# Kernel tuning notes

Hardware: AMD Instinct MI355X
Metric: run time of the kernel (lower is better)

## Reference

```python
import jax, jax.numpy as jnp
import numpy as np

N, E = 20000, 640000
F_IN, H, T = 64, 256, 64  # in_channels = T, edge_attr dim = T -> EdgeConv MLP in = 3*T


def _lin(key, fan_in, fan_out):
    k1, k2 = jax.random.split(key)
    s = 1.0 / np.sqrt(fan_in)
    W = jax.random.uniform(k1, (fan_in, fan_out), jnp.float32, -s, s)
    b = jax.random.uniform(k2, (fan_out,), jnp.float32, -s, s)
    return W, b


def setup_inputs() -> dict:
    key = jax.random.key(0)
    ks = jax.random.split(key, 12)
    x = jax.random.normal(ks[0], (N, F_IN), jnp.float32)
    edge_index = jax.random.randint(ks[1], (2, E), 0, N, jnp.int32)
    edge_attr = jax.random.normal(ks[2], (E, T), jnp.float32)
    conv1_W, conv1_b = _lin(ks[3], F_IN, H)
    e_W1, e_b1 = _lin(ks[4], 3 * T, H)
    e_W2, e_b2 = _lin(ks[5], H, H)
    conv2_W, conv2_b = _lin(ks[6], 2 * H, H)
    conv3_W, conv3_b = _lin(ks[7], H, F_IN)
    lin1_W, lin1_b = _lin(ks[8], 2 * F_IN, F_IN)
    lin2_W, lin2_b = _lin(ks[9], F_IN, 128)
    lin3_W, lin3_b = _lin(ks[10], 128, 32)
    lin4_W, lin4_b = _lin(ks[11], 32, 2)
    return dict(x=x, edge_index=edge_index, edge_attr=edge_attr,
                conv1_W=conv1_W, conv1_b=conv1_b,
                e_W1=e_W1, e_b1=e_b1, e_W2=e_W2, e_b2=e_b2,
                conv2_W=conv2_W, conv2_b=conv2_b,
                conv3_W=conv3_W, conv3_b=conv3_b,
                lin1_W=lin1_W, lin1_b=lin1_b, lin2_W=lin2_W, lin2_b=lin2_b,
                lin3_W=lin3_W, lin3_b=lin3_b, lin4_W=lin4_W, lin4_b=lin4_b)


def reference(x, edge_index, edge_attr,
              conv1_W, conv1_b, e_W1, e_b1, e_W2, e_b2,
              conv2_W, conv2_b, conv3_W, conv3_b,
              lin1_W, lin1_b, lin2_W, lin2_b, lin3_W, lin3_b, lin4_W, lin4_b):
    n = x.shape[0]
    src, dst = edge_index[0], edge_index[1]
    # GCN symmetric norm with self-loops (deg counted on dst, +1 for self-loop)
    deg = jax.ops.segment_sum(jnp.ones_like(src, jnp.float32), dst, num_segments=n) + 1.0
    dis = jax.lax.rsqrt(deg)

    def gcn(h, W, b):
        hw = h @ W
        msg = hw[src] * (dis[src] * dis[dst])[:, None]
        # self-loop contribution: norm = dis[i]^2
        return jax.ops.segment_sum(msg, dst, num_segments=n) + hw * (dis * dis)[:, None] + b

    out1 = jax.nn.relu(gcn(x, conv1_W, conv1_b))
    # EdgeConv: MLP(cat[x_i, x_j, edge_attr]) with max aggregation onto dst (x_i = target)
    m = jnp.concatenate([x[dst], x[src], edge_attr], axis=1)      # [E, 3T]
    m = jax.nn.relu(m @ e_W1 + e_b1) @ e_W2 + e_b2                 # [E, H]
    agg = jax.ops.segment_max(m, dst, num_segments=n)
    agg = jnp.where(jnp.isfinite(agg), agg, 0.0)                   # nodes with no in-edges
    out_e1 = jax.nn.relu(agg)

    out2 = jax.nn.relu(gcn(jnp.concatenate([out1, out_e1], axis=1), conv2_W, conv2_b))
    out3 = jax.nn.relu(gcn(out2, conv3_W, conv3_b))
    h = jnp.concatenate([x, out3], axis=1)
    h = jax.nn.softplus(h @ lin1_W + lin1_b)
    h = jax.nn.softplus(h @ lin2_W + lin2_b)
    h = jax.nn.softplus(h @ lin3_W + lin3_b)
    h = h @ lin4_W + lin4_b                                        # [N, 2]
    return (h[:, 0], h[:, 1])
```

## Files before the change

### kernel.cpp

```cpp
#include <hip/hip_runtime.h>
#include <stdint.h>

typedef __bf16 bf16x8 __attribute__((ext_vector_type(8)));
typedef float f32x4 __attribute__((ext_vector_type(4)));
typedef unsigned short u16x8 __attribute__((ext_vector_type(8)));
typedef unsigned long long ull_t;
typedef unsigned short ushort_t;

#define DEV __device__ __forceinline__

DEV unsigned short f2bf(float f) {
  __bf16 b = (__bf16)f;
  return __builtin_bit_cast(unsigned short, b);
}

DEV float bf2f(unsigned short b) { return __uint_as_float((unsigned int)b << 16); }

DEV f32x4 zero4() { f32x4 z = {0.f, 0.f, 0.f, 0.f}; return z; }

DEV float softplusf(float v) { return (v > 15.f) ? v : log1pf(expf(v)); }

DEV void pack_dev(const float* __restrict__ W, unsigned short* __restrict__ P,
                  int Ncols, int permk, int idx) {
  int j = idx & 7;
  int lane = (idx >> 3) & 63;
  int rest = idx >> 9;
  int NT = Ncols >> 4;
  int nt = rest % NT;
  int kt = rest / NT;
  int k = kt * 32 + ((j >> 2) * 16) + ((lane >> 4) * 4) + (j & 3);
  if (permk) k = (k & ~63) | ((k & 3) << 4) | ((k >> 2) & 15);
  int col = nt * 16 + (lane & 15);
  P[idx] = f2bf(W[(size_t)k * Ncols + col]);
}

__global__ __launch_bounds__(256) void k_prologue(
    const float* __restrict__ c1W, unsigned short* __restrict__ p_c1,
    const float* __restrict__ eW1, unsigned short* __restrict__ p_e1,
    const float* __restrict__ eW2, unsigned short* __restrict__ p_e2,
    const float* __restrict__ c2W, unsigned short* __restrict__ p_c2,
    const float* __restrict__ c3W, unsigned short* __restrict__ p_c3,
    const float* __restrict__ x, ushort_t* __restrict__ xb,
    const int* __restrict__ dsts, int* __restrict__ degi,
    int n4, int E, int nb_cvt) {
  const int b = blockIdx.x;
  const int tid = threadIdx.x;
  if (b < 64) {
    pack_dev(c1W, p_c1, 256, 0, b * 256 + tid);
  } else if (b < 256) {
    pack_dev(eW1, p_e1, 256, 0, (b - 64) * 256 + tid);
  } else if (b < 512) {
    pack_dev(eW2, p_e2, 256, 1, (b - 256) * 256 + tid);
  } else if (b < 1024) {
    pack_dev(c2W, p_c2, 256, 0, (b - 512) * 256 + tid);
  } else if (b < 1088) {
    pack_dev(c3W, p_c3, 64, 0, (b - 1024) * 256 + tid);
  } else if (b < 1088 + nb_cvt) {
    int i = (b - 1088) * 256 + tid;
    if (i < n4) {
      float4 v = *(const float4*)(x + (size_t)i * 4);
      ushort4 u;
      u.x = f2bf(v.x); u.y = f2bf(v.y); u.z = f2bf(v.z); u.w = f2bf(v.w);
      *(ushort4*)(xb + (size_t)i * 4) = u;
    }
  } else {
    int i = (b - 1088 - nb_cvt) * 256 + tid;
    if (i < E) atomicAdd(&degi[dsts[i]], 1);
  }
}

__global__ __launch_bounds__(1024) void k_scan_dis(const int* __restrict__ degi,
                                                   int* __restrict__ ptr,
                                                   float* __restrict__ dis, int n) {
  __shared__ int part[1024];
  const int tid = threadIdx.x;
  const int chunk = (n + 1023) / 1024;
  const int b = tid * chunk;
  const int e2 = min(n, b + chunk);
  int s = 0;
  for (int i = b; i < e2; ++i) {
    int d = degi[i];
    dis[i] = rsqrtf((float)d + 1.0f);
    s += d;
  }
  part[tid] = s;
  __syncthreads();
  for (int off = 1; off < 1024; off <<= 1) {
    int val = (tid >= off) ? part[tid - off] : 0;
    __syncthreads();
    part[tid] += val;
    __syncthreads();
  }
  int run = (tid == 0) ? 0 : part[tid - 1];
  for (int i = b; i < e2; ++i) {
    ptr[i] = run;
    run += degi[i];
  }
  if (tid == 1023) ptr[n] = run;
}

__global__ void k_fill(const int* __restrict__ srcs, const int* __restrict__ dsts,
                       const int* __restrict__ ptr, const float* __restrict__ dis,
                       int* __restrict__ fillc,
                       int2* __restrict__ sc_s, int* __restrict__ dst_s,
                       int* __restrict__ perm_s, int E) {
  int e = blockIdx.x * 256 + threadIdx.x;
  if (e >= E) return;
  int d = dsts[e];
  int s = srcs[e];
  int pos = ptr[d] + atomicAdd(&fillc[d], 1);
  float c = dis[s] * dis[d];
  sc_s[pos] = make_int2(s, __float_as_int(c));
  dst_s[pos] = d;
  perm_s[pos] = e;
}

template <int COLS, bool FINALIZE, bool INBF16>
__global__ __launch_bounds__(256) void k_gather_agg(
    const void* __restrict__ featv, const int2* __restrict__ sc,
    const int* __restrict__ ptr, const float* __restrict__ dis,
    const void* __restrict__ hwv, const float* __restrict__ bias,
    float* __restrict__ out, int n) {
  constexpr int V = COLS / 64;
  const int v = blockIdx.x * 4 + (threadIdx.x >> 6);
  if (v >= n) return;
  const int lane = threadIdx.x & 63;
  const int beg = ptr[v], end = ptr[v + 1];

  auto loadrow = [&](int s, float* f) {
    if constexpr (INBF16) {
      const ushort_t* feat = (const ushort_t*)featv;
      if constexpr (V == 4) {
        ushort4 u = *(const ushort4*)(feat + (size_t)s * COLS + lane * 4);
        f[0] = bf2f(u.x); f[1] = bf2f(u.y); f[2] = bf2f(u.z); f[3] = bf2f(u.w);
      } else {
        f[0] = bf2f(feat[(size_t)s * COLS + lane]);
      }
    } else {
      const float* feat = (const float*)featv;
      if constexpr (V == 4) {
        float4 q = *(const float4*)(feat + (size_t)s * COLS + lane * 4);
        f[0] = q.x; f[1] = q.y; f[2] = q.z; f[3] = q.w;
      } else {
        f[0] = feat[(size_t)s * COLS + lane];
      }
    }
  };

  float acc[V];
#pragma unroll
  for (int i = 0; i < V; ++i) acc[i] = 0.f;
  const int cnt = end - beg;
  const int2* scp = sc + beg;
  int i = 0;
  for (; i + 4 <= cnt; i += 4) {
    int2 s0 = scp[i], s1 = scp[i + 1], s2 = scp[i + 2], s3 = scp[i + 3];
    float f0[V], f1[V], f2[V], f3[V];
    loadrow(s0.x, f0); loadrow(s1.x, f1); loadrow(s2.x, f2); loadrow(s3.x, f3);
    float c0 = __int_as_float(s0.y), c1 = __int_as_float(s1.y);
    float c2 = __int_as_float(s2.y), c3 = __int_as_float(s3.y);
#pragma unroll
    for (int j = 0; j < V; ++j)
      acc[j] += f0[j] * c0 + f1[j] * c1 + f2[j] * c2 + f3[j] * c3;
  }
  for (; i < cnt; ++i) {
    int2 s0 = scp[i];
    float c0 = __int_as_float(s0.y);
    float f0[V];
    loadrow(s0.x, f0);
#pragma unroll
    for (int j = 0; j < V; ++j) acc[j] += f0[j] * c0;
  }
  float* op = out + (size_t)v * COLS + lane * V;
  if constexpr (FINALIZE) {
    const float dv = dis[v];
    float d2 = dv * dv;
    float h[V];
    if constexpr (INBF16) {
      const ushort_t* hw = (const ushort_t*)hwv;
      if constexpr (V == 4) {
        ushort4 u = *(const ushort4*)(hw + (size_t)v * COLS + lane * 4);
        h[0] = bf2f(u.x); h[1] = bf2f(u.y); h[2] = bf2f(u.z); h[3] = bf2f(u.w);
      } else {
        h[0] = bf2f(hw[(size_t)v * COLS + lane]);
      }
    } else {
      const float* hw = (const float*)hwv;
      if constexpr (V == 4) {
        float4 q = *(const float4*)(hw + (size_t)v * COLS + lane * 4);
        h[0] = q.x; h[1] = q.y; h[2] = q.z; h[3] = q.w;
      } else {
        h[0] = hw[(size_t)v * COLS + lane];
      }
    }
#pragma unroll
    for (int i2 = 0; i2 < V; ++i2)
      acc[i2] = fmaxf(acc[i2] + h[i2] * d2 + bias[lane * V + i2], 0.f);
  }
  if constexpr (V == 4) {
    *(float4*)op = make_float4(acc[0], acc[1], acc[2], acc[3]);
  } else {
    op[0] = acc[0];
  }
}

template <int K, int NOUT, bool COMPOSE, bool RELUBIAS, bool OUTBF16>
__global__ __launch_bounds__(256, 2) void gcn_gemm(
    const float* __restrict__ inA, const float* __restrict__ inB,
    const float* __restrict__ dis,
    const unsigned short* __restrict__ Wp, const float* __restrict__ bias,
    void* __restrict__ outv, int out_stride, int nrows) {
  constexpr int NT = NOUT / 16;
  constexpr int NTW = NOUT / 64;
  __shared__ unsigned short s_in[64 * K];
  const int tid = threadIdx.x;
  const int r0 = blockIdx.x * 64;

  constexpr int C4R = K / 4;
  for (int idx = tid; idx < 64 * C4R; idx += 256) {
    int row = idx / C4R;
    int rem = idx - row * C4R;
    int grow = r0 + row;
    float4 v = make_float4(0.f, 0.f, 0.f, 0.f);
    if (grow < nrows) {
      v = *(const float4*)&inA[(size_t)grow * K + rem * 4];
      if constexpr (COMPOSE) {
        float d = dis[grow];
        d *= d;
        float4 w2 = *(const float4*)&inB[(size_t)grow * K + rem * 4];
        v.x += w2.x * d; v.y += w2.y * d; v.z += w2.z * d; v.w += w2.w * d;
      }
    }
    ushort4 b;
    b.x = f2bf(v.x); b.y = f2bf(v.y); b.z = f2bf(v.z); b.w = f2bf(v.w);
    *(ushort4*)&s_in[row * K + ((rem ^ (row & 7)) * 4)] = b;
  }
  __syncthreads();

  const int lane = tid & 63, wid = tid >> 6;
  const int lr = lane & 15, lg = lane >> 4;
  f32x4 acc[4][NTW];
#pragma unroll
  for (int m = 0; m < 4; ++m)
#pragma unroll
    for (int n2 = 0; n2 < NTW; ++n2) acc[m][n2] = zero4();

#pragma unroll
  for (int kt = 0; kt < K / 32; ++kt) {
    bf16x8 a[4];
#pragma unroll
    for (int m = 0; m < 4; ++m) {
      int rA = m * 16 + lr;
      int c1 = (kt * 8 + lg) ^ (rA & 7);
      int c2 = (kt * 8 + lg + 4) ^ (rA & 7);
      union { bf16x8 v; ull_t q[2]; } u;
      u.q[0] = *(const ull_t*)&s_in[rA * K + c1 * 4];
      u.q[1] = *(const ull_t*)&s_in[rA * K + c2 * 4];
      a[m] = u.v;
    }
#pragma unroll
    for (int n2 = 0; n2 < NTW; ++n2) {
      int nt = wid * NTW + n2;
      bf16x8 b = *(const bf16x8*)&Wp[(((kt * NT + nt) * 64 + lane) * 8)];
#pragma unroll
      for (int m = 0; m < 4; ++m)
        acc[m][n2] = __builtin_amdgcn_mfma_f32_16x16x32_bf16(a[m], b, acc[m][n2], 0, 0, 0);
    }
  }

#pragma unroll
  for (int n2 = 0; n2 < NTW; ++n2) {
    int col = (wid * NTW + n2) * 16 + lr;
    float bv = 0.f;
    if (RELUBIAS) bv = bias[col];
#pragma unroll
    for (int m = 0; m < 4; ++m) {
#pragma unroll
      for (int r = 0; r < 4; ++r) {
        int grow = r0 + m * 16 + lg * 4 + r;
        if (grow < nrows) {
          float v = acc[m][n2][r];
          if (RELUBIAS) v = fmaxf(v + bv, 0.f);
          if constexpr (OUTBF16) {
            ((ushort_t*)outv)[(size_t)grow * out_stride + col] = f2bf(v);
          } else {
            ((float*)outv)[(size_t)grow * out_stride + col] = v;
          }
        }
      }
    }
  }
}

__global__ __launch_bounds__(512, 4) void k_fused(
    const float* __restrict__ x, const float* __restrict__ ea,
    const int2* __restrict__ sc_s, const int* __restrict__ dst_s,
    const int* __restrict__ perm_s,
    const unsigned short* __restrict__ W1p, const float* __restrict__ b1,
    const unsigned short* __restrict__ W2p, const float* __restrict__ b2,
    float* __restrict__ h2, int E, int nbE,
    const ushort_t* __restrict__ xb, const int* __restrict__ ptr,
    float* __restrict__ agg1, int n) {
  const int tid = threadIdx.x;
  const int lane = tid & 63, wid = tid >> 6;

  if (blockIdx.x >= nbE) {
    const int v = (blockIdx.x - nbE) * 8 + wid;
    if (v >= n) return;
    const int beg = ptr[v], end = ptr[v + 1];
    float acc = 0.f;
    const int cnt = end - beg;
    const int2* scp = sc_s + beg;
    int i = 0;
    for (; i + 4 <= cnt; i += 4) {
      int2 s0 = scp[i], s1 = scp[i + 1], s2 = scp[i + 2], s3 = scp[i + 3];
      float f0 = bf2f(xb[(size_t)s0.x * 64 + lane]);
      float f1 = bf2f(xb[(size_t)s1.x * 64 + lane]);
      float f2 = bf2f(xb[(size_t)s2.x * 64 + lane]);
      float f3 = bf2f(xb[(size_t)s3.x * 64 + lane]);
      acc += f0 * __int_as_float(s0.y) + f1 * __int_as_float(s1.y) +
             f2 * __int_as_float(s2.y) + f3 * __int_as_float(s3.y);
    }
    for (; i < cnt; ++i) {
      int2 s0 = scp[i];
      acc += bf2f(xb[(size_t)s0.x * 64 + lane]) * __int_as_float(s0.y);
    }
    agg1[(size_t)v * 64 + lane] = acc;
    return;
  }

  __shared__ unsigned short s_buf[256 * 136];
  __shared__ int s_src[128], s_dst[128], s_perm[128];
  __shared__ ull_t s_mask[2];
  const int e0 = blockIdx.x * 128;
  if (tid < 128) {
    int e = e0 + tid;
    s_src[tid] = (e < E) ? sc_s[e].x : 0;
    s_dst[tid] = (e < E) ? dst_s[e] : 0;
    s_perm[tid] = (e < E) ? perm_s[e] : 0;
  }
  __syncthreads();
  if (wid < 2) {
    int r = wid * 64 + lane;
    bool chg = (r > 0) && (s_dst[r] != s_dst[r - 1]);
    ull_t m = __ballot(chg);
    if (lane == 0) s_mask[wid] = m;
  }
#pragma unroll
  for (int seg = 0; seg < 3; ++seg) {
#pragma unroll
    for (int it = 0; it < 4; ++it) {
      int idx = it * 512 + tid;
      int ei = idx >> 4;
      int q = idx & 15;
      const float* row;
      if (seg == 0) row = x + (unsigned)s_dst[ei] * 64u;
      else if (seg == 1) row = x + (unsigned)s_src[ei] * 64u;
      else row = ea + (unsigned)s_perm[ei] * 64u;
      float4 v = make_float4(0.f, 0.f, 0.f, 0.f);
      if (e0 + ei < E) v = *(const float4*)(row + q * 4);
      ushort4 b;
      b.x = f2bf(v.x); b.y = f2bf(v.y); b.z = f2bf(v.z); b.w = f2bf(v.w);
      int chunk = (seg * 16 + q) ^ (ei & 7);
      *(ushort4*)&s_buf[ei * 192 + chunk * 4] = b;
    }
  }
  __syncthreads();

  const int wr = wid >> 2;
  const int wc = wid & 3;
  const int lr = lane & 15, lg = lane >> 4;
  f32x4 acc[4][4];
#pragma unroll
  for (int m = 0; m < 4; ++m)
#pragma unroll
    for (int n2 = 0; n2 < 4; ++n2) acc[m][n2] = zero4();

#pragma unroll
  for (int kt = 0; kt < 6; ++kt) {
    bf16x8 a[4];
#pragma unroll
    for (int m = 0; m < 4; ++m) {
      int rA = wr * 64 + m * 16 + lr;
      int rr = rA & 7;
      union { bf16x8 v; ull_t q[2]; } u;
      u.q[0] = *(const ull_t*)&s_buf[rA * 192 + ((kt * 8 + lg) ^ rr) * 4];
      u.q[1] = *(const ull_t*)&s_buf[rA * 192 + ((kt * 8 + lg + 4) ^ rr) * 4];
      a[m] = u.v;
    }
#pragma unroll
    for (int n2 = 0; n2 < 4; ++n2) {
      int nt = wc * 4 + n2;
      bf16x8 b = *(const bf16x8*)&W1p[(((kt * 16 + nt) * 64 + lane) * 8)];
#pragma unroll
      for (int m = 0; m < 4; ++m)
        acc[m][n2] = __builtin_amdgcn_mfma_f32_16x16x32_bf16(a[m], b, acc[m][n2], 0, 0, 0);
    }
  }
  __syncthreads();

  {
    float b1v[4];
#pragma unroll
    for (int n2 = 0; n2 < 4; ++n2) b1v[n2] = b1[(wc * 4 + n2) * 16 + lr];
#pragma unroll
    for (int m = 0; m < 4; ++m) {
#pragma unroll
      for (int r = 0; r < 4; ++r) {
        int row = wr * 64 + m * 16 + lg * 4 + r;
        union { ushort_t h[4]; ull_t q; } pk;
        pk.h[0] = f2bf(fmaxf(acc[m][0][r] + b1v[0], 0.f));
        pk.h[1] = f2bf(fmaxf(acc[m][1][r] + b1v[1], 0.f));
        pk.h[2] = f2bf(fmaxf(acc[m][2][r] + b1v[2], 0.f));
        pk.h[3] = f2bf(fmaxf(acc[m][3][r] + b1v[3], 0.f));
        int chunk = (wc * 16 + lr) ^ (row & 7);
        *(ull_t*)&s_buf[row * 256 + chunk * 4] = pk.q;
      }
    }
  }
  __syncthreads();

#pragma unroll
  for (int m = 0; m < 4; ++m)
#pragma unroll
    for (int n2 = 0; n2 < 4; ++n2) acc[m][n2] = zero4();
#pragma unroll
  for (int kt = 0; kt < 8; ++kt) {
    bf16x8 a[4];
#pragma unroll
    for (int m = 0; m < 4; ++m) {
      int rA = wr * 64 + m * 16 + lr;
      int rr = rA & 7;
      union { bf16x8 v; ull_t q[2]; } u;
      u.q[0] = *(const ull_t*)&s_buf[rA * 256 + ((kt * 8 + lg) ^ rr) * 4];
      u.q[1] = *(const ull_t*)&s_buf[rA * 256 + ((kt * 8 + lg + 4) ^ rr) * 4];
      a[m] = u.v;
    }
#pragma unroll
    for (int n2 = 0; n2 < 4; ++n2) {
      int nt = wc * 4 + n2;
      bf16x8 b = *(const bf16x8*)&W2p[(((kt * 16 + nt) * 64 + lane) * 8)];
#pragma unroll
      for (int m = 0; m < 4; ++m)
        acc[m][n2] = __builtin_amdgcn_mfma_f32_16x16x32_bf16(a[m], b, acc[m][n2], 0, 0, 0);
    }
  }
  __syncthreads();

#pragma unroll
  for (int n2 = 0; n2 < 4; ++n2) {
    int col = (wc * 4 + n2) * 16 + lr;
    float bv = b2[col];
#pragma unroll
    for (int m = 0; m < 4; ++m) {
      int rbase = wr * 64 + m * 16 + lg * 4;
      union { ushort_t h[4]; ull_t q; } pk;
#pragma unroll
      for (int r = 0; r < 4; ++r) {
        int row = rbase + r;
        float v = (e0 + row < E) ? fmaxf(acc[m][n2][r] + bv, 0.f) : 0.f;
        pk.h[r] = f2bf(v);
      }
      *(ull_t*)&s_buf[col * 136 + rbase] = pk.q;
    }
  }
  __syncthreads();

  {
    const int col = tid & 255;
    const int half = tid >> 8;
    const int rbeg = half * 64;
    const ull_t mask = s_mask[half];
    unsigned int run = 0;
    int segstart = rbeg;
#pragma unroll
    for (int i = 0; i < 8; ++i) {
      u16x8 pack = *(const u16x8*)&s_buf[col * 136 + rbeg + i * 8];
#pragma unroll
      for (int r2 = 0; r2 < 8; ++r2) {
        int rloc = i * 8 + r2;
        if ((mask >> rloc) & 1ull) {
          if (run > 0)
            atomicMax((int*)h2 + ((unsigned)s_dst[segstart] * 512u + 256u + col),
                      (int)(run << 16));
          run = 0;
          segstart = rbeg + rloc;
        }
        run = max(run, (unsigned int)pack[r2]);
      }
    }
    if (run > 0)
      atomicMax((int*)h2 + ((unsigned)s_dst[segstart] * 512u + 256u + col),
                (int)(run << 16));
  }
}

__global__ __launch_bounds__(256) void k_head(
    const float* __restrict__ x, const float* __restrict__ out3,
    const float* __restrict__ W1, const float* __restrict__ b1,
    const float* __restrict__ W2, const float* __restrict__ b2,
    const float* __restrict__ W3, const float* __restrict__ b3,
    const float* __restrict__ W4, const float* __restrict__ b4,
    float* __restrict__ out, int n) {
  __shared__ float sW1[128 * 64];
  __shared__ float sW3[128 * 32];
  __shared__ float sW4[32 * 2];
  __shared__ float sb1[64], sb2[128], sb3[32], sb4[2];
  __shared__ float sbuf[4][352];
  const int tid = threadIdx.x;
  for (int i = tid; i < 128 * 64; i += 256) sW1[i] = W1[i];
  for (int i = tid; i < 128 * 32; i += 256) sW3[i] = W3[i];
  if (tid < 64) sW4[tid] = W4[tid];
  if (tid < 64) sb1[tid] = b1[tid];
  if (tid < 128) sb2[tid] = b2[tid];
  if (tid < 32) sb3[tid] = b3[tid];
  if (tid < 2) sb4[tid] = b4[tid];
  __syncthreads();
  const int wid = tid >> 6, lane = tid & 63;
  float* B = sbuf[wid];
  const int per = gridDim.x * 4;
  const int iters = (n + per - 1) / per;
  for (int it = 0; it < iters; ++it) {
    const int node = it * per + blockIdx.x * 4 + wid;
    const bool act = node < n;
    if (act) {
      B[lane] = x[(size_t)node * 64 + lane];
      B[64 + lane] = out3[(size_t)node * 64 + lane];
    }
    __syncthreads();
    if (act) {
      float o = sb1[lane];
#pragma unroll 8
      for (int k = 0; k < 128; ++k) o += B[k] * sW1[k * 64 + lane];
      B[128 + lane] = softplusf(o);
    }
    __syncthreads();
    if (act) {
      float o0 = sb2[lane], o1 = sb2[64 + lane];
#pragma unroll 8
      for (int k = 0; k < 64; ++k) {
        float v = B[128 + k];
        o0 += v * W2[k * 128 + lane];
        o1 += v * W2[k * 128 + 64 + lane];
      }
      B[192 + lane] = softplusf(o0);
      B[256 + lane] = softplusf(o1);
    }
    __syncthreads();
    if (act && lane < 32) {
      float o = sb3[lane];
#pragma unroll 8
      for (int k = 0; k < 128; ++k) o += B[192 + k] * sW3[k * 32 + lane];
      B[320 + lane] = softplusf(o);
    }
    __syncthreads();
    if (act && lane < 2) {
      float o = sb4[lane];
#pragma unroll
      for (int k = 0; k < 32; ++k) o += B[320 + k] * sW4[k * 2 + lane];
      out[(size_t)lane * n + node] = o;
    }
    __syncthreads();
  }
}

static inline size_t alignup(size_t v) { return (v + 255) & ~(size_t)255; }

extern "C" void kernel_launch(void* const* d_in, const int* in_sizes, int n_in,
                              void* d_out, int out_size, void* d_ws, size_t ws_size,
                              hipStream_t stream) {
  const float* x = (const float*)d_in[0];
  const int* ei = (const int*)d_in[1];
  const float* ea = (const float*)d_in[2];
  const float* c1W = (const float*)d_in[3];
  const float* c1b = (const float*)d_in[4];
  const float* eW1 = (const float*)d_in[5];
  const float* eb1 = (const float*)d_in[6];
  const float* eW2 = (const float*)d_in[7];
  const float* eb2 = (const float*)d_in[8];
  const float* c2W = (const float*)d_in[9];
  const float* c2b = (const float*)d_in[10];
  const float* c3W = (const float*)d_in[11];
  const float* c3b = (const float*)d_in[12];
  const float* l1W = (const float*)d_in[13];
  const float* l1b = (const float*)d_in[14];
  const float* l2W = (const float*)d_in[15];
  const float* l2b = (const float*)d_in[16];
  const float* l3W = (const float*)d_in[17];
  const float* l3b = (const float*)d_in[18];
  const float* l4W = (const float*)d_in[19];
  const float* l4b = (const float*)d_in[20];
  const int n = in_sizes[0] / 64;
  const int E = in_sizes[1] / 2;
  const int* srcs = ei;
  const int* dsts = ei + E;

  char* w = (char*)d_ws;
  auto alloc = [&](size_t bytes) {
    char* p = w;
    w += alignup(bytes);
    return p;
  };
  float* dis = (float*)alloc((size_t)n * 4);
  int* degi = (int*)alloc((size_t)n * 4);
  int* ptr = (int*)alloc((size_t)(n + 1) * 4);
  int* fillc = (int*)alloc((size_t)n * 4);
  int2* sc_s = (int2*)alloc((size_t)E * 8);
  int* dst_s = (int*)alloc((size_t)E * 4);
  int* perm_s = (int*)alloc((size_t)E * 4);
  float* agg1 = (float*)alloc((size_t)n * 64 * 4);
  float* h2 = (float*)alloc((size_t)n * 512 * 4);
  ushort_t* hw2b = (ushort_t*)alloc((size_t)n * 256 * 2);
  float* out2 = (float*)alloc((size_t)n * 256 * 4);
  ushort_t* hw3b = (ushort_t*)alloc((size_t)n * 64 * 2);
  float* out3 = (float*)alloc((size_t)n * 64 * 4);
  ushort_t* xb = (ushort_t*)alloc((size_t)n * 64 * 2);
  unsigned short* p_c1 = (unsigned short*)alloc(64 * 256 * 2);
  unsigned short* p_e1 = (unsigned short*)alloc(192 * 256 * 2);
  unsigned short* p_e2 = (unsigned short*)alloc(256 * 256 * 2);
  unsigned short* p_c2 = (unsigned short*)alloc(512 * 256 * 2);
  unsigned short* p_c3 = (unsigned short*)alloc(256 * 64 * 2);

  hipMemsetAsync(degi, 0, (size_t)n * 4, stream);
  hipMemsetAsync(fillc, 0, (size_t)n * 4, stream);
  hipMemsetAsync(h2, 0, (size_t)n * 512 * 4, stream);

  const int n4 = n * 16;
  const int nb_cvt = (n4 + 255) / 256;
  const int nb_deg = (E + 255) / 256;
  k_prologue<<<1088 + nb_cvt + nb_deg, 256, 0, stream>>>(
      c1W, p_c1, eW1, p_e1, eW2, p_e2, c2W, p_c2, c3W, p_c3,
      x, xb, dsts, degi, n4, E, nb_cvt);

  k_scan_dis<<<1, 1024, 0, stream>>>(degi, ptr, dis, n);
  k_fill<<<(E + 255) / 256, 256, 0, stream>>>(srcs, dsts, ptr, dis, fillc,
                                              sc_s, dst_s, perm_s, E);

  const int ablocks = (n + 3) / 4;
  const int gblocks = (n + 63) / 64;
  const int nbE = (E + 127) / 128;
  const int nbG = (n + 7) / 8;

  k_fused<<<nbE + nbG, 512, 0, stream>>>(x, ea, sc_s, dst_s, perm_s,
                                         p_e1, eb1, p_e2, eb2, h2, E, nbE,
                                         xb, ptr, agg1, n);

  gcn_gemm<64, 256, true, true, false><<<gblocks, 256, 0, stream>>>(
      agg1, x, dis, p_c1, c1b, h2, 512, n);

  gcn_gemm<512, 256, false, false, true><<<gblocks, 256, 0, stream>>>(
      h2, nullptr, nullptr, p_c2, nullptr, hw2b, 256, n);
  k_gather_agg<256, true, true><<<ablocks, 256, 0, stream>>>(
      hw2b, sc_s, ptr, dis, hw2b, c2b, out2, n);

  gcn_gemm<256, 64, false, false, true><<<gblocks, 256, 0, stream>>>(
      out2, nullptr, nullptr, p_c3, nullptr, hw3b, 64, n);
  k_gather_agg<64, true, true><<<ablocks, 256, 0, stream>>>(
      hw3b, sc_s, ptr, dis, hw3b, c3b, out3, n);

  k_head<<<1250, 256, 0, stream>>>(x, out3, l1W, l1b, l2W, l2b, l3W, l3b, l4W, l4b,
                                   (float*)d_out, n);
}
```

Baseline: 617.2 us.

## Split h2 into bf16 GCN half and fp32 edge half, un-fuse agg kernel

Removes the side-branch from the fused EdgeConv kernel. The GCN-1 aggregation now runs as a separate k_gather_agg launch, and conv1 writes its output as bf16 into its own buffer. The EdgeConv atomics target a separate fp32 buffer half the former width, so the memset and traffic on the combined 512-wide fp32 h2 shrink. A new mixed-input GEMM reads the bf16 and fp32 halves and converts them while staging into shared memory. This adds a launch and gives up the overlap that came from co-scheduling the aggregation blocks with the edge blocks.

```diff
diff --git a/kernel.cpp b/kernel.cpp
--- a/kernel.cpp
+++ b/kernel.cpp
@@ -292,47 +292,91 @@
   }
 }
 
-__global__ __launch_bounds__(512, 4) void k_fused(
+__global__ __launch_bounds__(256, 2) void gcn_gemm_mix(
+    const ushort_t* __restrict__ h2a, const float* __restrict__ h2b,
+    const unsigned short* __restrict__ Wp, ushort_t* __restrict__ outv,
+    int nrows) {
+  constexpr int K = 512, NT = 16, NTW = 4;
+  __shared__ unsigned short s_in[64 * K];
+  const int tid = threadIdx.x;
+  const int r0 = blockIdx.x * 64;
+
+  for (int idx = tid; idx < 64 * 128; idx += 256) {
+    int row = idx >> 7;
+    int rem = idx & 127;
+    int grow = r0 + row;
+    ushort4 b = make_ushort4(0, 0, 0, 0);
+    if (grow < nrows) {
+      if (rem < 64) {
+        b = *(const ushort4*)&h2a[(size_t)grow * 256 + rem * 4];
+      } else {
+        float4 v = *(const float4*)&h2b[(size_t)grow * 256 + (rem - 64) * 4];
+        b.x = f2bf(v.x); b.y = f2bf(v.y); b.z = f2bf(v.z); b.w = f2bf(v.w);
+      }
+    }
+    *(ushort4*)&s_in[row * K + ((rem ^ (row & 7)) * 4)] = b;
+  }
+  __syncthreads();
+
+  const int lane = tid & 63, wid = tid >> 6;
+  const int lr = lane & 15, lg = lane >> 4;
+  f32x4 acc[4][NTW];
+#pragma unroll
+  for (int m = 0; m < 4; ++m)
+#pragma unroll
+    for (int n2 = 0; n2 < NTW; ++n2) acc[m][n2] = zero4();
+
+#pragma unroll
+  for (int kt = 0; kt < K / 32; ++kt) {
+    bf16x8 a[4];
+#pragma unroll
+    for (int m = 0; m < 4; ++m) {
+      int rA = m * 16 + lr;
+      int c1 = (kt * 8 + lg) ^ (rA & 7);
+      int c2 = (kt * 8 + lg + 4) ^ (rA & 7);
+      union { bf16x8 v; ull_t q[2]; } u;
+      u.q[0] = *(const ull_t*)&s_in[rA * K + c1 * 4];
+      u.q[1] = *(const ull_t*)&s_in[rA * K + c2 * 4];
+      a[m] = u.v;
+    }
+#pragma unroll
+    for (int n2 = 0; n2 < NTW; ++n2) {
+      int nt = wid * NTW + n2;
+      bf16x8 b = *(const bf16x8*)&Wp[(((kt * NT + nt) * 64 + lane) * 8)];
+#pragma unroll
+      for (int m = 0; m < 4; ++m)
+        acc[m][n2] = __builtin_amdgcn_mfma_f32_16x16x32_bf16(a[m], b, acc[m][n2], 0, 0, 0);
+    }
+  }
+
+#pragma unroll
+  for (int n2 = 0; n2 < NTW; ++n2) {
+    int col = (wid * NTW + n2) * 16 + lr;
+#pragma unroll
+    for (int m = 0; m < 4; ++m) {
+#pragma unroll
+      for (int r = 0; r < 4; ++r) {
+        int grow = r0 + m * 16 + lg * 4 + r;
+        if (grow < nrows)
+          outv[(size_t)grow * 256 + col] = f2bf(acc[m][n2][r]);
+      }
+    }
+  }
+}
+
+__global__ __launch_bounds__(512, 4) void k_edgeconv(
     const float* __restrict__ x, const float* __restrict__ ea,
     const int2* __restrict__ sc_s, const int* __restrict__ dst_s,
     const int* __restrict__ perm_s,
     const unsigned short* __restrict__ W1p, const float* __restrict__ b1,
     const unsigned short* __restrict__ W2p, const float* __restrict__ b2,
-    float* __restrict__ h2, int E, int nbE,
-    const ushort_t* __restrict__ xb, const int* __restrict__ ptr,
-    float* __restrict__ agg1, int n) {
-  const int tid = threadIdx.x;
-  const int lane = tid & 63, wid = tid >> 6;
-
-  if (blockIdx.x >= nbE) {
-    const int v = (blockIdx.x - nbE) * 8 + wid;
-    if (v >= n) return;
-    const int beg = ptr[v], end = ptr[v + 1];
-    float acc = 0.f;
-    const int cnt = end - beg;
-    const int2* scp = sc_s + beg;
-    int i = 0;
-    for (; i + 4 <= cnt; i += 4) {
-      int2 s0 = scp[i], s1 = scp[i + 1], s2 = scp[i + 2], s3 = scp[i + 3];
-      float f0 = bf2f(xb[(size_t)s0.x * 64 + lane]);
-      float f1 = bf2f(xb[(size_t)s1.x * 64 + lane]);
-      float f2 = bf2f(xb[(size_t)s2.x * 64 + lane]);
-      float f3 = bf2f(xb[(size_t)s3.x * 64 + lane]);
-      acc += f0 * __int_as_float(s0.y) + f1 * __int_as_float(s1.y) +
-             f2 * __int_as_float(s2.y) + f3 * __int_as_float(s3.y);
-    }
-    for (; i < cnt; ++i) {
-      int2 s0 = scp[i];
-      acc += bf2f(xb[(size_t)s0.x * 64 + lane]) * __int_as_float(s0.y);
-    }
-    agg1[(size_t)v * 64 + lane] = acc;
-    return;
-  }
-
+    float* __restrict__ h2b, int E) {
   __shared__ unsigned short s_buf[256 * 136];
   __shared__ int s_src[128], s_dst[128], s_perm[128];
   __shared__ ull_t s_mask[2];
+  const int tid = threadIdx.x;
   const int e0 = blockIdx.x * 128;
+  const int lane = tid & 63, wid = tid >> 6;
   if (tid < 128) {
     int e = e0 + tid;
     s_src[tid] = (e < E) ? sc_s[e].x : 0;
@@ -481,7 +525,7 @@
         int rloc = i * 8 + r2;
         if ((mask >> rloc) & 1ull) {
           if (run > 0)
-            atomicMax((int*)h2 + ((unsigned)s_dst[segstart] * 512u + 256u + col),
+            atomicMax((int*)h2b + ((unsigned)s_dst[segstart] * 256u + col),
                       (int)(run << 16));
           run = 0;
           segstart = rbeg + rloc;
@@ -490,7 +534,7 @@
       }
     }
     if (run > 0)
-      atomicMax((int*)h2 + ((unsigned)s_dst[segstart] * 512u + 256u + col),
+      atomicMax((int*)h2b + ((unsigned)s_dst[segstart] * 256u + col),
                 (int)(run << 16));
   }
 }
@@ -609,7 +653,8 @@
   int* dst_s = (int*)alloc((size_t)E * 4);
   int* perm_s = (int*)alloc((size_t)E * 4);
   float* agg1 = (float*)alloc((size_t)n * 64 * 4);
-  float* h2 = (float*)alloc((size_t)n * 512 * 4);
+  ushort_t* h2a = (ushort_t*)alloc((size_t)n * 256 * 2);
+  float* h2b = (float*)alloc((size_t)n * 256 * 4);
   ushort_t* hw2b = (ushort_t*)alloc((size_t)n * 256 * 2);
   float* out2 = (float*)alloc((size_t)n * 256 * 4);
   ushort_t* hw3b = (ushort_t*)alloc((size_t)n * 64 * 2);
@@ -623,7 +668,7 @@
 
   hipMemsetAsync(degi, 0, (size_t)n * 4, stream);
   hipMemsetAsync(fillc, 0, (size_t)n * 4, stream);
-  hipMemsetAsync(h2, 0, (size_t)n * 512 * 4, stream);
+  hipMemsetAsync(h2b, 0, (size_t)n * 256 * 4, stream);
 
   const int n4 = n * 16;
   const int nb_cvt = (n4 + 255) / 256;
@@ -638,18 +683,16 @@
 
   const int ablocks = (n + 3) / 4;
   const int gblocks = (n + 63) / 64;
-  const int nbE = (E + 127) / 128;
-  const int nbG = (n + 7) / 8;
-
-  k_fused<<<nbE + nbG, 512, 0, stream>>>(x, ea, sc_s, dst_s, perm_s,
-                                         p_e1, eb1, p_e2, eb2, h2, E, nbE,
-                                         xb, ptr, agg1, n);
-
-  gcn_gemm<64, 256, true, true, false><<<gblocks, 256, 0, stream>>>(
-      agg1, x, dis, p_c1, c1b, h2, 512, n);
-
-  gcn_gemm<512, 256, false, false, true><<<gblocks, 256, 0, stream>>>(
-      h2, nullptr, nullptr, p_c2, nullptr, hw2b, 256, n);
+
+  k_gather_agg<64, false, true><<<ablocks, 256, 0, stream>>>(
+      xb, sc_s, ptr, dis, nullptr, nullptr, agg1, n);
+  gcn_gemm<64, 256, true, true, true><<<gblocks, 256, 0, stream>>>(
+      agg1, x, dis, p_c1, c1b, h2a, 256, n);
+
+  k_edgeconv<<<(E + 127) / 128, 512, 0, stream>>>(x, ea, sc_s, dst_s, perm_s,
+                                                  p_e1, eb1, p_e2, eb2, h2b, E);
+
+  gcn_gemm_mix<<<gblocks, 256, 0, stream>>>(h2a, h2b, p_c2, hw2b, n);
   k_gather_agg<256, true, true><<<ablocks, 256, 0, stream>>>(
       hw2b, sc_s, ptr, dis, hw2b, c2b, out2, n);
 
```

After: 591.3 us. -4.2%, faster.
